# Performance work log

Measured on AMD Instinct MI355X. Metric: run time of the kernel, lower is better.

Reference implementation:

```python
import jax, jax.numpy as jnp
import numpy as np

N = 8192        # num_drugs
D_EMB = 256     # args.gcn_hidden3 (global encoder input)
D_FEAT = 256    # args.hidden_size (local encoder input)
H1 = H2 = H3 = 256  # args.ff_hidden1/2/3
LOG2 = float(np.log(2.0))
ADJ_DENSITY = 0.01


def _ff(x, w1, b1, w2, b2, w3, b3, ws, bs):
    # FF block: 3-layer ReLU MLP + linear shortcut (FF_local / FF_global)
    h = jax.nn.relu(x @ w1 + b1)
    h = jax.nn.relu(h @ w2 + b2)
    h = jax.nn.relu(h @ w3 + b3)
    return h + x @ ws + bs


def _lin_init(k, fan_in, fan_out):
    s = 1.0 / np.sqrt(fan_in)
    kw, kb = jax.random.split(k)
    w = jax.random.uniform(kw, (fan_in, fan_out), minval=-s, maxval=s, dtype=jnp.float32)
    b = jax.random.uniform(kb, (fan_out,), minval=-s, maxval=s, dtype=jnp.float32)
    return w, b


def setup_inputs() -> dict:
    key = jax.random.key(0)
    ks = jax.random.split(key, 11)
    g_w1, g_b1 = _lin_init(ks[0], D_EMB, H1)
    g_w2, g_b2 = _lin_init(ks[1], H1, H2)
    g_w3, g_b3 = _lin_init(ks[2], H2, H3)
    g_ws, g_bs = _lin_init(ks[3], D_EMB, H3)
    l_w1, l_b1 = _lin_init(ks[4], D_FEAT, H1)
    l_w2, l_b2 = _lin_init(ks[5], H1, H2)
    l_w3, l_b3 = _lin_init(ks[6], H2, H3)
    l_ws, l_bs = _lin_init(ks[7], D_FEAT, H3)
    embeddings = jax.random.normal(ks[8], (N, D_EMB), dtype=jnp.float32)
    features = jax.random.normal(ks[9], (N, D_FEAT), dtype=jnp.float32)
    adj_tensor = (jax.random.uniform(ks[10], (N, N)) < ADJ_DENSITY).astype(jnp.float32)
    return dict(embeddings=embeddings, features=features, adj_tensor=adj_tensor,
                num_drugs=N,
                g_w1=g_w1, g_b1=g_b1, g_w2=g_w2, g_b2=g_b2, g_w3=g_w3, g_b3=g_b3,
                g_ws=g_ws, g_bs=g_bs,
                l_w1=l_w1, l_b1=l_b1, l_w2=l_w2, l_b2=l_b2, l_w3=l_w3, l_b3=l_b3,
                l_ws=l_ws, l_bs=l_bs)


def reference(embeddings, features, adj_tensor,
              g_w1, g_b1, g_w2, g_b2, g_w3, g_b3, g_ws, g_bs,
              l_w1, l_b1, l_w2, l_b2, l_w3, l_b3, l_ws, l_bs,
              num_drugs):
    g_enc = _ff(embeddings, g_w1, g_b1, g_w2, g_b2, g_w3, g_b3, g_ws, g_bs)  # [N, H3]
    l_enc = _ff(features,   l_w1, l_b1, l_w2, l_b2, l_w3, l_b3, l_ws, l_bs)  # [N, H3]
    res = l_enc @ g_enc.T                      # [N, N] pairwise local-global scores
    pos_mask = adj_tensor
    neg_mask = 1.0 - adj_tensor
    # JSD estimator (as in InfoGraph/MIRACLE: mask applied BEFORE the expectation)
    p = res * pos_mask
    E_pos = jnp.sum(LOG2 - jax.nn.softplus(-p)) / num_drugs
    q = res * neg_mask
    E_neg = jnp.sum(jax.nn.softplus(-q) + q - LOG2) / (num_drugs * (num_drugs - 1))
    return E_neg - E_pos  # prior=False -> PRIOR term is 0
```

## Files before the change

kernel.cpp:

```cpp
#include <hip/hip_runtime.h>
#include <hip/hip_bf16.h>
#include <stdint.h>

typedef __bf16 bf16;
typedef __bf16 bf16x8 __attribute__((ext_vector_type(8)));
typedef float f32x4 __attribute__((ext_vector_type(4)));

#define N_DRUGS 8192
#define DIM 256
#define LOG2_C 0.6931471805599453f
#define W_POS (1.0f / 8192.0f)
#define W_NEG (1.0f / (8192.0f * 8191.0f))

__device__ inline void gload_lds16(const void* g, void* l) {
  __builtin_amdgcn_global_load_lds(
      (const __attribute__((address_space(1))) void*)g,
      (__attribute__((address_space(3))) void*)l, 16, 0, 0);
}

__device__ inline int swz(int row, int c) {
  return (c & ~7) | ((c ^ row) & 7);
}

__device__ inline float load_as_f32(const void* p, size_t idx, int dt_bf16) {
  return dt_bf16 ? (float)((const bf16*)p)[idx] : ((const float*)p)[idx];
}

__global__ void detect_dtype(const unsigned short* emb, int* flag) {
  int l = threadIdx.x & 63;
  unsigned short u = emb[2 * l];
  int e = (u >> 7) & 0xFF;
  int plausible = (e >= 96 && e <= 140) || (u == 0);
  unsigned long long m = __ballot(plausible);
  if (l == 0) *flag = (__popcll(m) >= 32) ? 1 : 0;
}

struct P8 { const void* p[8]; };

__global__ __launch_bounds__(256) void transpose_w(P8 srcs, bf16* wt,
                                                   const int* flag) {
  __shared__ bf16 t[32][33];
  const int dt = *flag;
  int m = blockIdx.z;
  const void* src = srcs.p[m];
  bf16* dst = wt + m * 65536;
  int bx = blockIdx.x * 32;
  int by = blockIdx.y * 32;
  int tx = threadIdx.x, ty = threadIdx.y;
#pragma unroll
  for (int i = 0; i < 32; i += 8)
    t[ty + i][tx] = (bf16)load_as_f32(src, (size_t)(by + ty + i) * DIM + bx + tx, dt);
  __syncthreads();
#pragma unroll
  for (int i = 0; i < 32; i += 8)
    dst[(bx + ty + i) * DIM + by + tx] = t[tx][ty + i];
}

struct FFArgs {
  const void *x, *b1, *b2, *b3, *bs;
  const bf16 *wt1, *wt2, *wt3, *wts;
  bf16* out;
};
struct FFBoth { FFArgs a[2]; };

__global__ __launch_bounds__(256) void ff_kernel(FFBoth both, const int* flag) {
  __shared__ __align__(16) bf16 xin[64 * 256];
  __shared__ __align__(16) bf16 cur[64 * 256];
  const FFArgs A = (blockIdx.y == 0) ? both.a[0] : both.a[1];
  const int dt = *flag;

  const int t = threadIdx.x;
  const int w = t >> 6, l = t & 63;
  const int lm = l & 15, lq = l >> 4;
  const int n0 = w * 64;
  const int r0 = blockIdx.x * 64;

  if (dt) {
#pragma unroll
    for (int it = 0; it < 8; ++it) {
      int ci = it * 256 + t, row = ci >> 5, c = ci & 31;
      *(bf16x8*)&xin[row * 256 + swz(row, c) * 8] =
          *(const bf16x8*)&((const bf16*)A.x)[(size_t)(r0 + row) * DIM + c * 8];
    }
  } else {
#pragma unroll
    for (int it = 0; it < 8; ++it) {
      int ci = it * 256 + t, row = ci >> 5, c = ci & 31;
      const float* src = &((const float*)A.x)[(size_t)(r0 + row) * DIM + c * 8];
      bf16x8 v;
#pragma unroll
      for (int e = 0; e < 8; ++e) v[e] = (bf16)src[e];
      *(bf16x8*)&xin[row * 256 + swz(row, c) * 8] = v;
    }
  }
  __syncthreads();

  f32x4 acc[4][4];
  const f32x4 fz = {0.f, 0.f, 0.f, 0.f};

  auto compute = [&](const bf16* src, const bf16* wt) {
#pragma unroll
    for (int i = 0; i < 4; ++i)
#pragma unroll
      for (int j = 0; j < 4; ++j) acc[i][j] = fz;
#pragma unroll
    for (int ks = 0; ks < 256; ks += 32) {
      bf16x8 af[4], bfr[4];
#pragma unroll
      for (int i = 0; i < 4; ++i) {
        int row = i * 16 + lm;
        int k = ks + lq * 8;
        af[i] = *(const bf16x8*)&src[row * 256 + swz(row, k >> 3) * 8];
      }
#pragma unroll
      for (int j = 0; j < 4; ++j) {
        int n = n0 + j * 16 + lm;
        bfr[j] = *(const bf16x8*)&wt[n * DIM + ks + lq * 8];
      }
#pragma unroll
      for (int i = 0; i < 4; ++i)
#pragma unroll
        for (int j = 0; j < 4; ++j)
          acc[i][j] = __builtin_amdgcn_mfma_f32_16x16x32_bf16(af[i], bfr[j],
                                                              acc[i][j], 0, 0, 0);
    }
  };

  auto store_relu = [&](const void* bias) {
    __syncthreads();
#pragma unroll
    for (int j = 0; j < 4; ++j) {
      int col = n0 + j * 16 + lm;
      float bj = load_as_f32(bias, col, dt);
      int cc = col >> 3, cw = col & 7;
#pragma unroll
      for (int i = 0; i < 4; ++i)
#pragma unroll
        for (int r = 0; r < 4; ++r) {
          int row = i * 16 + lq * 4 + r;
          float v = fmaxf(acc[i][j][r] + bj, 0.f);
          cur[row * 256 + swz(row, cc) * 8 + cw] = (bf16)v;
        }
    }
    __syncthreads();
  };

  compute(xin, A.wt1); store_relu(A.b1);
  compute(cur, A.wt2); store_relu(A.b2);
  compute(cur, A.wt3); store_relu(A.b3);
  compute(xin, A.wts);

#pragma unroll
  for (int j = 0; j < 4; ++j) {
    int col = n0 + j * 16 + lm;
    float bj = load_as_f32(A.bs, col, dt);
    int cc = col >> 3, cw = col & 7;
#pragma unroll
    for (int i = 0; i < 4; ++i)
#pragma unroll
      for (int r = 0; r < 4; ++r) {
        int row = i * 16 + lq * 4 + r;
        float h3 = (float)cur[row * 256 + swz(row, cc) * 8 + cw];
        float v = acc[i][j][r] + bj + h3;
        A.out[(size_t)(r0 + row) * DIM + col] = (bf16)v;
      }
  }
}

__global__ __launch_bounds__(256) void gemm_reduce(const bf16* __restrict__ Lenc,
                                                   const bf16* __restrict__ Genc,
                                                   const void* __restrict__ adj,
                                                   float* accum, const int* flag) {
  __shared__ __align__(16) bf16 At[128 * 64];
  __shared__ __align__(16) bf16 Bt[128 * 64];
  __shared__ float red[256];

  const int dt = *flag;
  const int t = threadIdx.x;
  const int w = t >> 6, l = t & 63;
  const int wr = w >> 1, wc = w & 1;
  const int lm = l & 15, lq = l >> 4;
  const int row0 = blockIdx.y * 128;
  const int col0 = blockIdx.x * 128;

  f32x4 acc[4][4];
  const f32x4 fz = {0.f, 0.f, 0.f, 0.f};
#pragma unroll
  for (int i = 0; i < 4; ++i)
#pragma unroll
    for (int j = 0; j < 4; ++j) acc[i][j] = fz;

  for (int kk = 0; kk < 256; kk += 64) {
    __syncthreads();
#pragma unroll
    for (int it = 0; it < 4; ++it) {
      int ci = it * 256 + t;
      int row = ci >> 3, cs = ci & 7;
      int cg = swz(row, cs);
      bf16* lbase = &At[(it * 256 + w * 64) * 8];
      gload_lds16(&Lenc[(size_t)(row0 + row) * DIM + kk + cg * 8], lbase);
      bf16* lbase2 = &Bt[(it * 256 + w * 64) * 8];
      gload_lds16(&Genc[(size_t)(col0 + row) * DIM + kk + cg * 8], lbase2);
    }
    __syncthreads();
#pragma unroll
    for (int ks = 0; ks < 64; ks += 32) {
      bf16x8 af[4], bfr[4];
#pragma unroll
      for (int i = 0; i < 4; ++i) {
        int row = wr * 64 + i * 16 + lm;
        int kc = (ks >> 3) + lq;
        af[i] = *(const bf16x8*)&At[row * 64 + swz(row, kc) * 8];
      }
#pragma unroll
      for (int j = 0; j < 4; ++j) {
        int row = wc * 64 + j * 16 + lm;
        int kc = (ks >> 3) + lq;
        bfr[j] = *(const bf16x8*)&Bt[row * 64 + swz(row, kc) * 8];
      }
#pragma unroll
      for (int i = 0; i < 4; ++i)
#pragma unroll
        for (int j = 0; j < 4; ++j)
          acc[i][j] = __builtin_amdgcn_mfma_f32_16x16x32_bf16(af[i], bfr[j],
                                                              acc[i][j], 0, 0, 0);
    }
  }

  float lsum = 0.f;
#pragma unroll
  for (int i = 0; i < 4; ++i) {
#pragma unroll
    for (int r = 0; r < 4; ++r) {
      int rr = row0 + wr * 64 + i * 16 + lq * 4 + r;
      size_t abase = (size_t)rr * N_DRUGS + col0 + wc * 64;
#pragma unroll
      for (int j = 0; j < 4; ++j) {
        float res = acc[i][j][r];
        float a = load_as_f32(adj, abase + j * 16 + lm, dt);
        float s = fmaxf(res, 0.f) + __logf(1.f + __expf(-fabsf(res)));
        float vneg = (s - LOG2_C) * W_NEG;
        float vpos = (s - res - LOG2_C) * W_POS;
        lsum += (a > 0.5f) ? vpos : vneg;
      }
    }
  }

  red[t] = lsum;
  __syncthreads();
#pragma unroll
  for (int sft = 128; sft > 0; sft >>= 1) {
    if (t < sft) red[t] += red[t + sft];
    __syncthreads();
  }
  if (t == 0) atomicAdd(accum, red[0]);
}

__global__ void finalize_k(const float* accum, unsigned int* out) {
  if (threadIdx.x == 0 && blockIdx.x == 0) {
    float v = *accum;
    union { bf16 h; unsigned short u; } cv;
    cv.h = (bf16)v;
    out[0] = ((unsigned int)cv.u << 16) | cv.u;
  }
}

extern "C" void kernel_launch(void* const* d_in, const int* in_sizes, int n_in,
                              void* d_out, int out_size, void* d_ws, size_t ws_size,
                              hipStream_t stream) {
  const void* embeddings = d_in[0];
  const void* features   = d_in[1];
  const void* adj        = d_in[2];

  char* ws = (char*)d_ws;
  float* accum = (float*)ws;
  int* flag = (int*)(ws + 64);
  bf16* wt   = (bf16*)(ws + 1024);
  bf16* genc = (bf16*)(ws + 1024 + 8 * 65536 * 2);
  bf16* lenc = (bf16*)(ws + 1024 + 8 * 65536 * 2 + (size_t)N_DRUGS * DIM * 2);

  hipMemsetAsync(accum, 0, sizeof(float), stream);

  detect_dtype<<<1, 64, 0, stream>>>((const unsigned short*)embeddings, flag);

  P8 srcs;
  srcs.p[0] = d_in[4];  srcs.p[1] = d_in[6];  srcs.p[2] = d_in[8];  srcs.p[3] = d_in[10];
  srcs.p[4] = d_in[12]; srcs.p[5] = d_in[14]; srcs.p[6] = d_in[16]; srcs.p[7] = d_in[18];
  transpose_w<<<dim3(8, 8, 8), dim3(32, 8), 0, stream>>>(srcs, wt, flag);

  FFBoth fb;
  fb.a[0] = FFArgs{embeddings, d_in[5], d_in[7], d_in[9], d_in[11],
                   wt + 0 * 65536, wt + 1 * 65536, wt + 2 * 65536, wt + 3 * 65536,
                   genc};
  fb.a[1] = FFArgs{features, d_in[13], d_in[15], d_in[17], d_in[19],
                   wt + 4 * 65536, wt + 5 * 65536, wt + 6 * 65536, wt + 7 * 65536,
                   lenc};
  ff_kernel<<<dim3(128, 2), 256, 0, stream>>>(fb, flag);

  gemm_reduce<<<dim3(64, 64), 256, 0, stream>>>(lenc, genc, adj, accum, flag);

  finalize_k<<<1, 64, 0, stream>>>(accum, (unsigned int*)d_out);
}
```

Measured before the change: 460.2 us.

## Stage adjacency tiles through LDS with coalesced loads and use wave-shuffle reduction

The epilogue of the pairwise GEMM previously read the adjacency mask directly from global memory in the MFMA fragment layout, giving strided, poorly coalesced loads. It now stages each adjacency tile into the reused GEMM shared memory through swizzled 16-byte global-to-LDS loads, handling fp32 in two halves, and reads values back in fragment order. The block reduction becomes a wave shuffle plus a 4-entry shared array. Separately, the FF kernel is widened to 512 threads with each wave owning 32 output columns, which adds parallelism but halves per-wave reuse of activation fragments.

Measured after the change: 455.2 us. About the same (-1.1%).

```diff
diff --git a/kernel.cpp b/kernel.cpp
--- a/kernel.cpp
+++ b/kernel.cpp
@@ -63,7 +63,7 @@
 };
 struct FFBoth { FFArgs a[2]; };
 
-__global__ __launch_bounds__(256) void ff_kernel(FFBoth both, const int* flag) {
+__global__ __launch_bounds__(512) void ff_kernel(FFBoth both, const int* flag) {
   __shared__ __align__(16) bf16 xin[64 * 256];
   __shared__ __align__(16) bf16 cur[64 * 256];
   const FFArgs A = (blockIdx.y == 0) ? both.a[0] : both.a[1];
@@ -72,20 +72,20 @@
   const int t = threadIdx.x;
   const int w = t >> 6, l = t & 63;
   const int lm = l & 15, lq = l >> 4;
-  const int n0 = w * 64;
+  const int n0 = w * 32;
   const int r0 = blockIdx.x * 64;
 
   if (dt) {
 #pragma unroll
-    for (int it = 0; it < 8; ++it) {
-      int ci = it * 256 + t, row = ci >> 5, c = ci & 31;
+    for (int it = 0; it < 4; ++it) {
+      int ci = it * 512 + t, row = ci >> 5, c = ci & 31;
       *(bf16x8*)&xin[row * 256 + swz(row, c) * 8] =
           *(const bf16x8*)&((const bf16*)A.x)[(size_t)(r0 + row) * DIM + c * 8];
     }
   } else {
 #pragma unroll
-    for (int it = 0; it < 8; ++it) {
-      int ci = it * 256 + t, row = ci >> 5, c = ci & 31;
+    for (int it = 0; it < 4; ++it) {
+      int ci = it * 512 + t, row = ci >> 5, c = ci & 31;
       const float* src = &((const float*)A.x)[(size_t)(r0 + row) * DIM + c * 8];
       bf16x8 v;
 #pragma unroll
@@ -95,32 +95,31 @@
   }
   __syncthreads();
 
-  f32x4 acc[4][4];
+  f32x4 acc[4][2];
   const f32x4 fz = {0.f, 0.f, 0.f, 0.f};
 
   auto compute = [&](const bf16* src, const bf16* wt) {
 #pragma unroll
     for (int i = 0; i < 4; ++i)
 #pragma unroll
-      for (int j = 0; j < 4; ++j) acc[i][j] = fz;
+      for (int j = 0; j < 2; ++j) acc[i][j] = fz;
 #pragma unroll
     for (int ks = 0; ks < 256; ks += 32) {
-      bf16x8 af[4], bfr[4];
+      bf16x8 af[4], bfr[2];
 #pragma unroll
       for (int i = 0; i < 4; ++i) {
         int row = i * 16 + lm;
-        int k = ks + lq * 8;
-        af[i] = *(const bf16x8*)&src[row * 256 + swz(row, k >> 3) * 8];
-      }
-#pragma unroll
-      for (int j = 0; j < 4; ++j) {
+        af[i] = *(const bf16x8*)&src[row * 256 + swz(row, (ks >> 3) + lq) * 8];
+      }
+#pragma unroll
+      for (int j = 0; j < 2; ++j) {
         int n = n0 + j * 16 + lm;
         bfr[j] = *(const bf16x8*)&wt[n * DIM + ks + lq * 8];
       }
 #pragma unroll
       for (int i = 0; i < 4; ++i)
 #pragma unroll
-        for (int j = 0; j < 4; ++j)
+        for (int j = 0; j < 2; ++j)
           acc[i][j] = __builtin_amdgcn_mfma_f32_16x16x32_bf16(af[i], bfr[j],
                                                               acc[i][j], 0, 0, 0);
     }
@@ -129,7 +128,7 @@
   auto store_relu = [&](const void* bias) {
     __syncthreads();
 #pragma unroll
-    for (int j = 0; j < 4; ++j) {
+    for (int j = 0; j < 2; ++j) {
       int col = n0 + j * 16 + lm;
       float bj = load_as_f32(bias, col, dt);
       int cc = col >> 3, cw = col & 7;
@@ -151,7 +150,7 @@
   compute(xin, A.wts);
 
 #pragma unroll
-  for (int j = 0; j < 4; ++j) {
+  for (int j = 0; j < 2; ++j) {
     int col = n0 + j * 16 + lm;
     float bj = load_as_f32(A.bs, col, dt);
     int cc = col >> 3, cw = col & 7;
@@ -171,9 +170,10 @@
                                                    const bf16* __restrict__ Genc,
                                                    const void* __restrict__ adj,
                                                    float* accum, const int* flag) {
-  __shared__ __align__(16) bf16 At[128 * 64];
-  __shared__ __align__(16) bf16 Bt[128 * 64];
-  __shared__ float red[256];
+  __shared__ __align__(16) bf16 smem[2 * 128 * 64];
+  __shared__ float red[8];
+  bf16* At = smem;
+  bf16* Bt = smem + 128 * 64;
 
   const int dt = *flag;
   const int t = threadIdx.x;
@@ -209,14 +209,12 @@
 #pragma unroll
       for (int i = 0; i < 4; ++i) {
         int row = wr * 64 + i * 16 + lm;
-        int kc = (ks >> 3) + lq;
-        af[i] = *(const bf16x8*)&At[row * 64 + swz(row, kc) * 8];
+        af[i] = *(const bf16x8*)&At[row * 64 + swz(row, (ks >> 3) + lq) * 8];
       }
 #pragma unroll
       for (int j = 0; j < 4; ++j) {
         int row = wc * 64 + j * 16 + lm;
-        int kc = (ks >> 3) + lq;
-        bfr[j] = *(const bf16x8*)&Bt[row * 64 + swz(row, kc) * 8];
+        bfr[j] = *(const bf16x8*)&Bt[row * 64 + swz(row, (ks >> 3) + lq) * 8];
       }
 #pragma unroll
       for (int i = 0; i < 4; ++i)
@@ -228,32 +226,79 @@
   }
 
   float lsum = 0.f;
-#pragma unroll
-  for (int i = 0; i < 4; ++i) {
-#pragma unroll
-    for (int r = 0; r < 4; ++r) {
-      int rr = row0 + wr * 64 + i * 16 + lq * 4 + r;
-      size_t abase = (size_t)rr * N_DRUGS + col0 + wc * 64;
-#pragma unroll
-      for (int j = 0; j < 4; ++j) {
-        float res = acc[i][j][r];
-        float a = load_as_f32(adj, abase + j * 16 + lm, dt);
-        float s = fmaxf(res, 0.f) + __logf(1.f + __expf(-fabsf(res)));
-        float vneg = (s - LOG2_C) * W_NEG;
-        float vpos = (s - res - LOG2_C) * W_POS;
-        lsum += (a > 0.5f) ? vpos : vneg;
-      }
-    }
-  }
-
-  red[t] = lsum;
   __syncthreads();
-#pragma unroll
-  for (int sft = 128; sft > 0; sft >>= 1) {
-    if (t < sft) red[t] += red[t + sft];
-    __syncthreads();
-  }
-  if (t == 0) atomicAdd(accum, red[0]);
+
+  auto jsd = [&](float res, float a) {
+    float s = fmaxf(res, 0.f) + __logf(1.f + __expf(-fabsf(res)));
+    float vneg = (s - LOG2_C) * W_NEG;
+    float vpos = (s - res - LOG2_C) * W_POS;
+    return (a > 0.5f) ? vpos : vneg;
+  };
+
+  if (dt) {
+    const bf16* adjB = (const bf16*)adj;
+#pragma unroll
+    for (int it = 0; it < 8; ++it) {
+      int ci = it * 256 + t;
+      int row = ci >> 4, c = ci & 15;
+      int cg = c ^ (row & 15);
+      bf16* lbase = &smem[(it * 256 + w * 64) * 8];
+      gload_lds16(&adjB[(size_t)(row0 + row) * N_DRUGS + col0 + cg * 8], lbase);
+    }
+    __syncthreads();
+#pragma unroll
+    for (int i = 0; i < 4; ++i)
+#pragma unroll
+      for (int r = 0; r < 4; ++r) {
+        int row = wr * 64 + i * 16 + lq * 4 + r;
+#pragma unroll
+        for (int j = 0; j < 4; ++j) {
+          int col = wc * 64 + j * 16 + lm;
+          int slot = (col >> 3) ^ (row & 15);
+          float a = (float)smem[(row * 16 + slot) * 8 + (col & 7)];
+          lsum += jsd(acc[i][j][r], a);
+        }
+      }
+  } else {
+    const float* adjF = (const float*)adj;
+    float* AdjL = (float*)smem;
+    for (int h = 0; h < 2; ++h) {
+      if (h) __syncthreads();
+#pragma unroll
+      for (int it = 0; it < 8; ++it) {
+        int ci = it * 256 + t;
+        int r4 = ci >> 5, c = ci & 31;
+        int pr = (r4 >> 5) * 64 + h * 32 + (r4 & 31);
+        int cg = (c & 16) | ((c ^ (r4 & 15)) & 15);
+        float* lbase = &AdjL[(it * 256 + w * 64) * 4];
+        gload_lds16(&adjF[(size_t)(row0 + pr) * N_DRUGS + col0 + cg * 4], lbase);
+      }
+      __syncthreads();
+#pragma unroll
+      for (int ii = 0; ii < 2; ++ii) {
+        int i = 2 * h + ii;
+#pragma unroll
+        for (int r = 0; r < 4; ++r) {
+          int r4 = wr * 32 + ii * 16 + lq * 4 + r;
+#pragma unroll
+          for (int j = 0; j < 4; ++j) {
+            int col = wc * 64 + j * 16 + lm;
+            int cread = col >> 2;
+            int slot = (cread & 16) | ((cread ^ (r4 & 15)) & 15);
+            float a = AdjL[(r4 * 32 + slot) * 4 + (col & 3)];
+            lsum += jsd(acc[i][j][r], a);
+          }
+        }
+      }
+      if (h == 0) __syncthreads();
+    }
+  }
+
+#pragma unroll
+  for (int off = 32; off > 0; off >>= 1) lsum += __shfl_down(lsum, off, 64);
+  if (l == 0) red[w] = lsum;
+  __syncthreads();
+  if (t == 0) atomicAdd(accum, red[0] + red[1] + red[2] + red[3]);
 }
 
 __global__ void finalize_k(const float* accum, unsigned int* out) {
@@ -295,7 +340,7 @@
   fb.a[1] = FFArgs{features, d_in[13], d_in[15], d_in[17], d_in[19],
                    wt + 4 * 65536, wt + 5 * 65536, wt + 6 * 65536, wt + 7 * 65536,
                    lenc};
-  ff_kernel<<<dim3(128, 2), 256, 0, stream>>>(fb, flag);
+  ff_kernel<<<dim3(128, 2), 512, 0, stream>>>(fb, flag);
 
   gemm_reduce<<<dim3(64, 64), 256, 0, stream>>>(lenc, genc, adj, accum, flag);
 
```
